# Kernel optimization log

Measured on AMD Instinct MI355X. Metric: run time of the kernel, lower is better.

## Reference

```python
import jax, jax.numpy as jnp
import numpy as np

B, S, D = 32, 4096, 1024

def setup_inputs() -> dict:
    key = jax.random.key(0)
    k1, k2, k3, k4 = jax.random.split(key, 4)
    scale = 1.0 / np.sqrt(D)
    return {
        "dec_output": jax.random.normal(k1, (B, D), dtype=jnp.float32),
        "enc_outputs": jax.random.normal(k2, (B, S, D), dtype=jnp.float32),
        "W_in": jax.random.normal(k3, (D, D), dtype=jnp.float32) * scale,
        "W_out": jax.random.normal(k4, (D, 2 * D), dtype=jnp.float32) * scale,
    }

def reference(dec_output, enc_outputs, W_in, W_out):
    # dec_att = linear_in(dec_output): [B, D]  (nn.Linear: x @ W.T)
    dec_att = dec_output @ W_in.T
    # scores = bmm(enc_outputs, dec_att[:, :, None]).squeeze(2): [B, S]
    weights = jnp.einsum('bsd,bd->bs', enc_outputs, dec_att)
    # softmax over sourceL (no mask: self.mask is None)
    weights = jax.nn.softmax(weights, axis=-1)
    # weighted = bmm(weights[:, None, :], enc_outputs).squeeze(1): [B, D]
    weighted = jnp.einsum('bs,bsd->bd', weights, enc_outputs)
    combined = jnp.concatenate([weighted, dec_output], axis=1)  # [B, 2D]
    output = jnp.tanh(combined @ W_out.T)  # [B, D]
    return (output, weights)
```

## Files before the change

### kernel.cpp

```cpp
#include <hip/hip_runtime.h>
#include <math.h>

#define BB 32
#define SS 4096
#define DD 1024
#define SEGS 32
#define ROWS_PER_SEG (SS / SEGS)
#define GROUPS (ROWS_PER_SEG / 8)
#define NBLK2 (BB * SEGS)

typedef float vf4 __attribute__((ext_vector_type(4)));

__device__ __forceinline__ float wave_reduce_sum(float v) {
    #pragma unroll
    for (int off = 32; off > 0; off >>= 1)
        v += __shfl_xor(v, off, 64);
    return v;
}

__device__ __forceinline__ float dot4v(vf4 a, vf4 b) {
    return a.x * b.x + a.y * b.y + a.z * b.z + a.w * b.w;
}

__global__ __launch_bounds__(256) void k1_decatt(const float* __restrict__ dec,
                                                 const float* __restrict__ Win,
                                                 float* __restrict__ dec_att) {
    const int wid = threadIdx.x >> 6, lane = threadIdx.x & 63;
    const int d = blockIdx.x * 4 + wid;
    const vf4* Wrow = (const vf4*)(Win + (size_t)d * DD);
    vf4 w4[4];
    #pragma unroll
    for (int i = 0; i < 4; ++i) w4[i] = __builtin_nontemporal_load(&Wrow[lane + i * 64]);
    #pragma unroll 1
    for (int bg = 0; bg < 8; ++bg) {
        float p[4] = {0.f, 0.f, 0.f, 0.f};
        #pragma unroll
        for (int j = 0; j < 4; ++j) {
            const vf4* x = (const vf4*)(dec + (size_t)(bg * 4 + j) * DD);
            #pragma unroll
            for (int i = 0; i < 4; ++i) p[j] += dot4v(w4[i], x[lane + i * 64]);
        }
        #pragma unroll
        for (int off = 32; off > 0; off >>= 1) {
            #pragma unroll
            for (int j = 0; j < 4; ++j) p[j] += __shfl_xor(p[j], off, 64);
        }
        if (lane == 0) {
            #pragma unroll
            for (int j = 0; j < 4; ++j)
                dec_att[(size_t)(bg * 4 + j) * DD + d] = p[j];
        }
    }
}

__global__ __launch_bounds__(256) void k2_scan(const float* __restrict__ enc,
                                               const float* __restrict__ dec_att,
                                               float* __restrict__ scores,
                                               float* __restrict__ pacc,
                                               float* __restrict__ pml) {
    const int tid = threadIdx.x;
    const int wid = tid >> 6, lane = tid & 63;
    const int b = blockIdx.x / SEGS, seg = blockIdx.x % SEGS;
    const int s0 = seg * ROWS_PER_SEG;

    const vf4* encc = (const vf4*)(enc + ((size_t)b * SS + s0) * DD) + tid;
    const vf4 q4 = ((const vf4*)(dec_att + (size_t)b * DD))[tid];
    float* scores_row = scores + (size_t)b * SS + s0;

    vf4 a4 = (vf4)(0.f);
    float m = -1e30f, l = 0.f;

    __shared__ __align__(16) float lds_p[2][8][4];

    vf4 eC[8], eN[8];
    #pragma unroll
    for (int j = 0; j < 8; ++j)
        eC[j] = __builtin_nontemporal_load(&encc[(size_t)j * (DD / 4)]);

    auto process = [&](int g, const vf4* e) {
        float p[8];
        #pragma unroll
        for (int j = 0; j < 8; ++j) p[j] = dot4v(q4, e[j]);
        #pragma unroll
        for (int off = 32; off > 0; off >>= 1) {
            #pragma unroll
            for (int j = 0; j < 8; ++j) p[j] += __shfl_xor(p[j], off, 64);
        }
        if (lane == 0) {
            #pragma unroll
            for (int j = 0; j < 8; ++j) lds_p[g & 1][j][wid] = p[j];
        }
        asm volatile("s_waitcnt lgkmcnt(0)" ::: "memory");
        __builtin_amdgcn_s_barrier();
        float s[8];
        #pragma unroll
        for (int j = 0; j < 8; ++j) {
            const vf4 v = *(const vf4*)&lds_p[g & 1][j][0];
            s[j] = (v.x + v.y) + (v.z + v.w);
        }
        if (tid == 0) {
            #pragma unroll
            for (int j = 0; j < 8; ++j) scores_row[g * 8 + j] = s[j];
        }
        float mp = s[0];
        #pragma unroll
        for (int j = 1; j < 8; ++j) mp = fmaxf(mp, s[j]);
        const float mn = fmaxf(m, mp);
        const float sc = __expf(m - mn);
        float w[8], lsum = 0.f;
        #pragma unroll
        for (int j = 0; j < 8; ++j) { w[j] = __expf(s[j] - mn); lsum += w[j]; }
        l = l * sc + lsum;
        a4 *= sc;
        #pragma unroll
        for (int j = 0; j < 8; ++j) a4 += w[j] * e[j];
        m = mn;
    };

    #pragma unroll 1
    for (int g = 0; g < GROUPS - 1; ++g) {
        #pragma unroll
        for (int j = 0; j < 8; ++j)
            eN[j] = __builtin_nontemporal_load(&encc[(size_t)((g + 1) * 8 + j) * (DD / 4)]);
        process(g, eC);
        #pragma unroll
        for (int j = 0; j < 8; ++j) eC[j] = eN[j];
    }
    process(GROUPS - 1, eC);

    ((vf4*)(pacc + (size_t)blockIdx.x * DD))[tid] = a4;
    if (tid == 0) {
        pml[(size_t)blockIdx.x * 2 + 0] = m;
        pml[(size_t)blockIdx.x * 2 + 1] = l;
    }
}

__global__ __launch_bounds__(64) void k3_combine(const float* __restrict__ pacc,
                                                 const float* __restrict__ pml,
                                                 float* __restrict__ weighted,
                                                 float* __restrict__ wts) {
    const int b = blockIdx.x >> 2, qtr = blockIdx.x & 3;
    const int col = qtr * 64 + threadIdx.x;
    float mg = -1e30f;
    #pragma unroll 8
    for (int c = 0; c < SEGS; ++c) mg = fmaxf(mg, pml[(size_t)(b * SEGS + c) * 2]);
    float lg = 0.f;
    #pragma unroll 8
    for (int c = 0; c < SEGS; ++c)
        lg += pml[(size_t)(b * SEGS + c) * 2 + 1] * __expf(pml[(size_t)(b * SEGS + c) * 2] - mg);
    vf4 acc = (vf4)(0.f);
    #pragma unroll 4
    for (int c = 0; c < SEGS; ++c) {
        const float f = __expf(pml[(size_t)(b * SEGS + c) * 2] - mg);
        const vf4 v = __builtin_nontemporal_load(
            &((const vf4*)(pacc + (size_t)(b * SEGS + c) * DD))[col]);
        acc += f * v;
    }
    const float inv = 1.f / lg;
    ((vf4*)(weighted + (size_t)b * DD))[col] = acc * inv;

    vf4* wq = (vf4*)(wts + (size_t)b * SS + qtr * (SS / 4));
    #pragma unroll
    for (int i = 0; i < 4; ++i) {
        vf4 v = wq[threadIdx.x + i * 64];
        v.x = __expf(v.x - mg) * inv;
        v.y = __expf(v.y - mg) * inv;
        v.z = __expf(v.z - mg) * inv;
        v.w = __expf(v.w - mg) * inv;
        wq[threadIdx.x + i * 64] = v;
    }
}

__global__ __launch_bounds__(256) void k5_out(const float* __restrict__ weighted,
                                              const float* __restrict__ dec,
                                              const float* __restrict__ Wout,
                                              float* __restrict__ out) {
    const int wid = threadIdx.x >> 6, lane = threadIdx.x & 63;
    const int d = blockIdx.x * 4 + wid;
    const vf4* Wrow = (const vf4*)(Wout + (size_t)d * (2 * DD));
    vf4 w4[8];
    #pragma unroll
    for (int i = 0; i < 8; ++i) w4[i] = __builtin_nontemporal_load(&Wrow[lane + i * 64]);
    #pragma unroll 1
    for (int bg = 0; bg < 8; ++bg) {
        float p[4] = {0.f, 0.f, 0.f, 0.f};
        #pragma unroll
        for (int j = 0; j < 4; ++j) {
            const int b = bg * 4 + j;
            const vf4* xw = (const vf4*)(weighted + (size_t)b * DD);
            const vf4* xd = (const vf4*)(dec + (size_t)b * DD);
            #pragma unroll
            for (int i = 0; i < 4; ++i) {
                p[j] += dot4v(w4[i], xw[lane + i * 64]);
                p[j] += dot4v(w4[i + 4], xd[lane + i * 64]);
            }
        }
        #pragma unroll
        for (int off = 32; off > 0; off >>= 1) {
            #pragma unroll
            for (int j = 0; j < 4; ++j) p[j] += __shfl_xor(p[j], off, 64);
        }
        if (lane == 0) {
            #pragma unroll
            for (int j = 0; j < 4; ++j)
                out[(size_t)(bg * 4 + j) * DD + d] = tanhf(p[j]);
        }
    }
}

extern "C" void kernel_launch(void* const* d_in, const int* in_sizes, int n_in,
                              void* d_out, int out_size, void* d_ws, size_t ws_size,
                              hipStream_t stream) {
    (void)in_sizes; (void)n_in; (void)out_size; (void)ws_size;
    const float* dec  = (const float*)d_in[0];
    const float* enc  = (const float*)d_in[1];
    const float* Win  = (const float*)d_in[2];
    const float* Wout = (const float*)d_in[3];

    float* out_final = (float*)d_out;
    float* out_wts   = out_final + (size_t)BB * DD;

    float* ws       = (float*)d_ws;
    float* dec_att  = ws;
    float* pacc     = dec_att + (size_t)BB * DD;
    float* pml      = pacc + (size_t)NBLK2 * DD;
    float* weighted = pml + (size_t)NBLK2 * 2;

    hipLaunchKernelGGL(k1_decatt, dim3(DD / 4), dim3(256), 0, stream, dec, Win, dec_att);
    hipLaunchKernelGGL(k2_scan, dim3(NBLK2), dim3(256), 0, stream, enc, dec_att, out_wts, pacc, pml);
    hipLaunchKernelGGL(k3_combine, dim3(BB * 4), dim3(64), 0, stream, pacc, pml, weighted, out_wts);
    hipLaunchKernelGGL(k5_out, dim3(DD / 4), dim3(256), 0, stream, weighted, dec, Wout, out_final);
}
```

Baseline: 121.7 us.

## Fuse split-softmax combine into scan kernel via last-block atomic counter

Removes the separate combine kernel by having each scan block bump a per-batch atomic counter, and the last block for that batch does the cross-segment max/sum merge, writes the weighted vector and rescales the score row. This saves one kernel launch and its dependency gap. In exchange a memset launch is added, and the combine work for each batch now runs on a single 256-thread block at the tail of the scan.

```diff
diff --git a/kernel.cpp b/kernel.cpp
--- a/kernel.cpp
+++ b/kernel.cpp
@@ -57,7 +57,9 @@
                                                const float* __restrict__ dec_att,
                                                float* __restrict__ scores,
                                                float* __restrict__ pacc,
-                                               float* __restrict__ pml) {
+                                               float* __restrict__ pml,
+                                               float* __restrict__ weighted,
+                                               int* __restrict__ counters) {
     const int tid = threadIdx.x;
     const int wid = tid >> 6, lane = tid & 63;
     const int b = blockIdx.x / SEGS, seg = blockIdx.x % SEGS;
@@ -133,14 +135,17 @@
         pml[(size_t)blockIdx.x * 2 + 0] = m;
         pml[(size_t)blockIdx.x * 2 + 1] = l;
     }
-}
-
-__global__ __launch_bounds__(64) void k3_combine(const float* __restrict__ pacc,
-                                                 const float* __restrict__ pml,
-                                                 float* __restrict__ weighted,
-                                                 float* __restrict__ wts) {
-    const int b = blockIdx.x >> 2, qtr = blockIdx.x & 3;
-    const int col = qtr * 64 + threadIdx.x;
+
+    __threadfence();
+    __shared__ int lastflag;
+    if (tid == 0) {
+        const int old = atomicAdd(&counters[b], 1);
+        lastflag = (old == SEGS - 1) ? 1 : 0;
+    }
+    __syncthreads();
+    if (lastflag == 0) return;
+    __threadfence();
+
     float mg = -1e30f;
     #pragma unroll 8
     for (int c = 0; c < SEGS; ++c) mg = fmaxf(mg, pml[(size_t)(b * SEGS + c) * 2]);
@@ -152,22 +157,21 @@
     #pragma unroll 4
     for (int c = 0; c < SEGS; ++c) {
         const float f = __expf(pml[(size_t)(b * SEGS + c) * 2] - mg);
-        const vf4 v = __builtin_nontemporal_load(
-            &((const vf4*)(pacc + (size_t)(b * SEGS + c) * DD))[col]);
-        acc += f * v;
+        acc += f * __builtin_nontemporal_load(
+            &((const vf4*)(pacc + (size_t)(b * SEGS + c) * DD))[tid]);
     }
     const float inv = 1.f / lg;
-    ((vf4*)(weighted + (size_t)b * DD))[col] = acc * inv;
-
-    vf4* wq = (vf4*)(wts + (size_t)b * SS + qtr * (SS / 4));
+    ((vf4*)(weighted + (size_t)b * DD))[tid] = acc * inv;
+
+    vf4* wrow = (vf4*)(scores + (size_t)b * SS);
     #pragma unroll
     for (int i = 0; i < 4; ++i) {
-        vf4 v = wq[threadIdx.x + i * 64];
+        vf4 v = wrow[tid + i * 256];
         v.x = __expf(v.x - mg) * inv;
         v.y = __expf(v.y - mg) * inv;
         v.z = __expf(v.z - mg) * inv;
         v.w = __expf(v.w - mg) * inv;
-        wq[threadIdx.x + i * 64] = v;
+        wrow[tid + i * 256] = v;
     }
 }
 
@@ -225,9 +229,12 @@
     float* pacc     = dec_att + (size_t)BB * DD;
     float* pml      = pacc + (size_t)NBLK2 * DD;
     float* weighted = pml + (size_t)NBLK2 * 2;
+    int*   counters = (int*)(weighted + (size_t)BB * DD);
+
+    hipMemsetAsync(counters, 0, BB * sizeof(int), stream);
 
     hipLaunchKernelGGL(k1_decatt, dim3(DD / 4), dim3(256), 0, stream, dec, Win, dec_att);
-    hipLaunchKernelGGL(k2_scan, dim3(NBLK2), dim3(256), 0, stream, enc, dec_att, out_wts, pacc, pml);
-    hipLaunchKernelGGL(k3_combine, dim3(BB * 4), dim3(64), 0, stream, pacc, pml, weighted, out_wts);
+    hipLaunchKernelGGL(k2_scan, dim3(NBLK2), dim3(256), 0, stream,
+                       enc, dec_att, out_wts, pacc, pml, weighted, counters);
     hipLaunchKernelGGL(k5_out, dim3(DD / 4), dim3(256), 0, stream, weighted, dec, Wout, out_final);
 }
```

Measured after the change: 378.8 us. 211% more time.
